# Performance work log

Measured on AMD Instinct MI355X. Metric: run time of the kernel, lower is better.

## Reference

```python
import jax, jax.numpy as jnp
import numpy as np
from jax import lax

VOCAB, HIDDEN, LAYERS = 32000, 1024, 4
DT = 0.1


def setup_inputs() -> dict:
    key = jax.random.key(0)
    ks = jax.random.split(key, 12)
    B, S, H, L, V = 4, 512, HIDDEN, LAYERS, VOCAB
    xav = float(np.sqrt(6.0 / (H + H)))  # xavier_uniform bound for HxH
    # orthogonal-ish fixed W per layer (QR of gaussian)
    g = jax.random.normal(ks[0], (L, H, H), dtype=jnp.float32)
    Ws = jnp.stack([jnp.linalg.qr(g[i])[0] for i in range(L)])
    return {
        "input_ids": jax.random.randint(ks[1], (B, S), 0, V),
        "emb": jax.random.normal(ks[2], (V, H), dtype=jnp.float32) * 0.02,
        "proj_w": jax.random.normal(ks[3], (V, H), dtype=jnp.float32) * 0.02,
        "proj_b": jnp.zeros((V,), dtype=jnp.float32),
        "lambda_param": jnp.float32(0.0),
        "Ws": Ws,
        "Us": jax.random.uniform(ks[4], (L, H, H), jnp.float32, -xav, xav),
        "bs": jnp.zeros((L, H), dtype=jnp.float32),
        "tau_wh": jax.random.uniform(ks[5], (L, H, H), jnp.float32, -xav, xav),
        "tau_wu": jax.random.uniform(ks[6], (L, H, H), jnp.float32, -xav, xav),
        "tau_b": jax.random.uniform(ks[7], (L, H), jnp.float32, -2.0, 2.0),
    }


def reference(input_ids, emb, proj_w, proj_b, lambda_param, Ws, Us, bs, tau_wh, tau_wu, tau_b):
    L = Ws.shape[0]
    B, S = input_ids.shape
    H = emb.shape[1]
    x = emb[input_ids]  # [B, S, H]
    pos_lambda = jax.nn.softplus(lambda_param)

    def step(h, u_t):  # h: [L, B, H], u_t: [B, H]
        layer_in = u_t
        new_h = []
        for i in range(L):
            hp = h[i]
            tau = jax.nn.softplus(hp @ tau_wh[i].T + layer_in @ tau_wu[i].T + tau_b[i]) + 0.01
            tau = lax.stop_gradient(tau)  # torch.no_grad block
            act = jnp.tanh(hp @ Ws[i].T + layer_in @ Us[i].T + bs[i])
            dx = jnp.clip(pos_lambda * (-hp / tau + act), -10.0, 10.0)
            hn = hp + DT * dx
            new_h.append(hn)
            layer_in = hn
        return jnp.stack(new_h), layer_in

    h0 = jnp.zeros((L, B, H), dtype=x.dtype)
    hT, outs = lax.scan(step, h0, jnp.swapaxes(x, 0, 1))  # outs: [S, B, H]
    out_seq = jnp.swapaxes(outs, 0, 1)  # [B, S, H]
    logits = out_seq @ proj_w.T + proj_b  # [B, S, V]
    return logits, hT
```

## Files before the change

kernel.cpp:

```cpp
#include <hip/hip_runtime.h>
#include <hip/hip_bf16.h>

#define NL 4
#define NB 4
#define NS 512
#define NH 1024
#define NV 32000
#define RING 16

typedef unsigned int u32;
typedef unsigned short u16;
typedef __attribute__((ext_vector_type(8))) __bf16 vbf16x8;
typedef __attribute__((ext_vector_type(8))) u16   vu16x8;
typedef __attribute__((ext_vector_type(4))) u32   vu32x4;
typedef __attribute__((ext_vector_type(4))) float vf32x4;

__device__ __forceinline__ u16 f2bf(float f) {
    u32 x = __builtin_bit_cast(u32, f);
    x += 0x7FFFu + ((x >> 16) & 1u);
    return (u16)(x >> 16);
}
__device__ __forceinline__ float softplus_f(float x) {
    return fmaxf(x, 0.0f) + log1pf(expf(-fabsf(x)));
}
__device__ __forceinline__ int aloadi(const int* p) {
    return __hip_atomic_load(p, __ATOMIC_RELAXED, __HIP_MEMORY_SCOPE_AGENT);
}
__device__ __forceinline__ u32 aload32(const u32* p) {
    return __hip_atomic_load(p, __ATOMIC_RELAXED, __HIP_MEMORY_SCOPE_AGENT);
}
__device__ __forceinline__ void astorei(int* p, int v) {
    __hip_atomic_store(p, v, __ATOMIC_RELAXED, __HIP_MEMORY_SCOPE_AGENT);
}
__device__ __forceinline__ void astore32(u32* p, u32 v) {
    __hip_atomic_store(p, v, __ATOMIC_RELAXED, __HIP_MEMORY_SCOPE_AGENT);
}

#define APAD 8
#define ASTR (NH + APAD)

__global__ __launch_bounds__(256, 1) void lnn_recur(
    const int* __restrict__ ids, const float* __restrict__ emb,
    const float* __restrict__ Ws, const float* __restrict__ Us,
    const float* __restrict__ bsv, const float* __restrict__ twh,
    const float* __restrict__ twu, const float* __restrict__ tbv,
    const float* __restrict__ lambda_p,
    int* ack, u32* ring, u16* out16, float* hT_out)
{
    __shared__ __align__(16) u16 act_hp[5][ASTR];
    __shared__ __align__(16) u16 act_in[5][ASTR];
    __shared__ float cross[4][16][4];
    __shared__ float bias_a[16], bias_t[16];

    const int bid   = blockIdx.x;
    const int layer = bid & 3;
    const int slice = bid >> 2;
    const int j0    = slice << 4;
    const int tid   = threadIdx.x;
    const int wave  = tid >> 6;
    const int lane  = tid & 63;

    const float* msel = (wave == 0) ? Ws : (wave == 1) ? Us : (wave == 2) ? twh : twu;
    const float* mat  = msel + (size_t)layer * NH * NH;
    const int jr = j0 + (lane & 15);
    const int kb = (lane >> 4) * 8;
    vbf16x8 wfrag[32];
#pragma unroll
    for (int c = 0; c < 32; ++c) {
        const float* s = mat + (size_t)jr * NH + c * 32 + kb;
        vu16x8 t8;
#pragma unroll
        for (int e = 0; e < 8; ++e) t8[e] = f2bf(s[e]);
        wfrag[c] = __builtin_bit_cast(vbf16x8, t8);
    }

    for (int i = tid; i < ASTR; i += 256) { act_hp[4][i] = 0; act_in[4][i] = 0; }
    if (tid < 16) {
        bias_a[tid] = bsv[layer * NH + j0 + tid];
        bias_t[tid] = tbv[layer * NH + j0 + tid];
    }
    const float lam = softplus_f(lambda_p[0]);
    float hreg = 0.0f;
    const int lm1 = (layer > 0) ? layer - 1 : 0;

    for (int t = 0; t < NS; ++t) {
        {
            const int b = wave;
            const u32* hb_ = ring + (((size_t)(layer * NB + b)) * RING + ((t - 1) & (RING - 1))) * NH + lane;
            const u32* ib_ = ring + (((size_t)(lm1   * NB + b)) * RING + ( t      & (RING - 1))) * NH + lane;
            u32 hv[16], iv[16];
            u32 pendH = (t > 0)     ? 0xFFFFu : 0u;
            u32 pendI = (layer > 0) ? 0xFFFFu : 0u;
            const u32 seqH = (u32)t, seqI = (u32)(t + 1);
            const bool needAck = (wave == 0) && (layer < 3) && (t >= RING);
            const int  ackTgt  = t - RING + 1;
            const int* ackp    = ack + (layer + 1) * 64 + lane;
            bool ackok = !needAck;

            if (t == 0) {
#pragma unroll
                for (int i = 0; i < 16; ++i) hv[i] = 0;
            }
            if (layer == 0) {
                const int v = ids[b * NS + t];
                const float* er = emb + (size_t)v * NH + lane;
#pragma unroll
                for (int i = 0; i < 16; ++i) iv[i] = ((u32)f2bf(er[64 * i])) << 16;
            }
            for (int it = 0; it < (1 << 20); ++it) {
#pragma unroll
                for (int i = 0; i < 16; ++i) if (pendH & (1u << i)) hv[i] = aload32(hb_ + 64 * i);
#pragma unroll
                for (int i = 0; i < 16; ++i) if (pendI & (1u << i)) iv[i] = aload32(ib_ + 64 * i);
#pragma unroll
                for (int i = 0; i < 16; ++i) if ((pendH & (1u << i)) && ((hv[i] & 0xFFFFu) == seqH)) pendH &= ~(1u << i);
#pragma unroll
                for (int i = 0; i < 16; ++i) if ((pendI & (1u << i)) && ((iv[i] & 0xFFFFu) == seqI)) pendI &= ~(1u << i);
                if (needAck && !ackok) ackok = (aloadi(ackp) >= ackTgt);
                const bool done = (pendH == 0u) & (pendI == 0u) & (ackok | !needAck);
                if (__all((int)done)) break;
                __builtin_amdgcn_s_sleep(2);
            }
#pragma unroll
            for (int i = 0; i < 16; ++i) {
                act_hp[b][64 * i + lane] = (u16)(hv[i] >> 16);
                act_in[b][64 * i + lane] = (u16)(iv[i] >> 16);
            }
        }
        __syncthreads();
        if (tid == 0 && layer > 0) astorei(ack + layer * 64 + slice, t + 1);

        {
            const u16 (*asrc)[ASTR] = ((wave & 1) == 0) ? act_hp : act_in;
            int ar = lane & 15; if (ar > 4) ar = 4;
            vf32x4 a0 = {0.f,0.f,0.f,0.f}, a1 = a0, a2 = a0, a3 = a0;
#pragma unroll
            for (int c = 0; c < 32; c += 4) {
                a0 = __builtin_amdgcn_mfma_f32_16x16x32_bf16(*(const vbf16x8*)&asrc[ar][(c+0)*32+kb], wfrag[c+0], a0, 0, 0, 0);
                a1 = __builtin_amdgcn_mfma_f32_16x16x32_bf16(*(const vbf16x8*)&asrc[ar][(c+1)*32+kb], wfrag[c+1], a1, 0, 0, 0);
                a2 = __builtin_amdgcn_mfma_f32_16x16x32_bf16(*(const vbf16x8*)&asrc[ar][(c+2)*32+kb], wfrag[c+2], a2, 0, 0, 0);
                a3 = __builtin_amdgcn_mfma_f32_16x16x32_bf16(*(const vbf16x8*)&asrc[ar][(c+3)*32+kb], wfrag[c+3], a3, 0, 0, 0);
            }
            vf32x4 acc = (a0 + a1) + (a2 + a3);
            if (lane < 16) {
#pragma unroll
                for (int r = 0; r < 4; ++r) cross[wave][lane][r] = acc[r];
            }
        }
        __syncthreads();

        if (wave == 0) {
            const int j = lane & 15, b = lane >> 4;
            const float sa = cross[0][j][b] + cross[1][j][b] + bias_a[j];
            const float st = cross[2][j][b] + cross[3][j][b] + bias_t[j];
            const float tau = softplus_f(st) + 0.01f;
            const float av  = tanhf(sa);
            float dx = lam * (av - hreg / tau);
            dx = fminf(10.0f, fmaxf(-10.0f, dx));
            hreg = fmaf(0.1f, dx, hreg);
            const u16 hb = f2bf(hreg);
            const u32 pk = ((u32)hb << 16) | (u32)(t + 1);
            astore32(ring + (((size_t)(layer * NB + b)) * RING + (t & (RING - 1))) * NH + j0 + j, pk);
            if (layer == 3) out16[((size_t)b * NS + t) * NH + j0 + j] = hb;
            if (t == NS - 1) hT_out[((size_t)layer * NB + b) * NH + j0 + j] = hreg;
        }
    }
}

#define BM 128
#define BN 128
#define BK 32
#define KSTEPS (NH / BK)
#define LSTR (BK + 8)

__global__ __launch_bounds__(256, 1) void proj_gemm(
    const u16* __restrict__ A, const float* __restrict__ Bw,
    const float* __restrict__ bias, float* __restrict__ C)
{
    __shared__ __align__(16) u16 Asm[2][BM][LSTR];
    __shared__ __align__(16) u16 Bsm[2][BN][LSTR];

    const int tid  = threadIdx.x;
    const int wave = tid >> 6, lane = tid & 63;
    const int wr = wave >> 1, wc = wave & 1;

    const int nwg = gridDim.x;
    const int id  = blockIdx.x;
    const int q = nwg >> 3, r = nwg & 7;
    const int x = id & 7, o = id >> 3;
    const int wg = (x < r ? x * (q + 1) : r * (q + 1) + (x - r) * q) + o;
    const int m0 = (wg & 15) * BM;
    const int n0 = (wg >> 4) * BN;

    const int srow  = tid >> 1;
    const int shalf = tid & 1;
    const u16*   agp = A  + (size_t)(m0 + srow) * NH + shalf * 16;
    const float* bgp = Bw + (size_t)(n0 + srow) * NH + shalf * 16;

    vf32x4 zed = {0.f, 0.f, 0.f, 0.f};
    vf32x4 acc[4][4];
#pragma unroll
    for (int m = 0; m < 4; ++m)
#pragma unroll
        for (int n = 0; n < 4; ++n) acc[m][n] = zed;

    vu32x4 areg0, areg1; vf32x4 breg0, breg1, breg2, breg3;
    auto load_tile = [&](int kt) {
        const u16* ap = agp + kt * BK;
        areg0 = *(const vu32x4*)ap;
        areg1 = *(const vu32x4*)(ap + 8);
        const float* bp = bgp + kt * BK;
        breg0 = *(const vf32x4*)bp;       breg1 = *(const vf32x4*)(bp + 4);
        breg2 = *(const vf32x4*)(bp + 8); breg3 = *(const vf32x4*)(bp + 12);
    };
    auto write_tile = [&](int buf) {
        u16* ad = &Asm[buf][srow][shalf * 16];
        *(vu32x4*)ad = areg0; *(vu32x4*)(ad + 8) = areg1;
        float fb[16];
        *(vf32x4*)&fb[0] = breg0; *(vf32x4*)&fb[4]  = breg1;
        *(vf32x4*)&fb[8] = breg2; *(vf32x4*)&fb[12] = breg3;
        vu16x8 v0, v1;
#pragma unroll
        for (int e = 0; e < 8; ++e) { v0[e] = f2bf(fb[e]); v1[e] = f2bf(fb[8 + e]); }
        u16* bd = &Bsm[buf][srow][shalf * 16];
        *(vu16x8*)bd = v0; *(vu16x8*)(bd + 8) = v1;
    };

    load_tile(0); write_tile(0);
    __syncthreads();

    const int fr = lane & 15;
    const int fk = (lane >> 4) * 8;
    for (int kt = 0; kt < KSTEPS; ++kt) {
        const int cur = kt & 1;
        if (kt + 1 < KSTEPS) load_tile(kt + 1);
        vbf16x8 afr[4], bfr[4];
#pragma unroll
        for (int m = 0; m < 4; ++m)
            afr[m] = *(const vbf16x8*)&Asm[cur][wr * 64 + m * 16 + fr][fk];
#pragma unroll
        for (int n = 0; n < 4; ++n)
            bfr[n] = *(const vbf16x8*)&Bsm[cur][wc * 64 + n * 16 + fr][fk];
#pragma unroll
        for (int m = 0; m < 4; ++m)
#pragma unroll
            for (int n = 0; n < 4; ++n)
                acc[m][n] = __builtin_amdgcn_mfma_f32_16x16x32_bf16(afr[m], bfr[n], acc[m][n], 0, 0, 0);
        if (kt + 1 < KSTEPS) write_tile(cur ^ 1);
        __syncthreads();
    }

    const int cc = lane & 15;
    const int cr = (lane >> 4) * 4;
#pragma unroll
    for (int m = 0; m < 4; ++m) {
#pragma unroll
        for (int n = 0; n < 4; ++n) {
            const int gc = n0 + wc * 64 + n * 16 + cc;
            const float bval = bias[gc];
            float* cp = C + (size_t)(m0 + wr * 64 + m * 16 + cr) * NV + gc;
#pragma unroll
            for (int r = 0; r < 4; ++r)
                cp[(size_t)r * NV] = acc[m][n][r] + bval;
        }
    }
}

extern "C" void kernel_launch(void* const* d_in, const int* in_sizes, int n_in,
                              void* d_out, int out_size, void* d_ws, size_t ws_size,
                              hipStream_t stream) {
    const int*   ids = (const int*)  d_in[0];
    const float* emb = (const float*)d_in[1];
    const float* pw  = (const float*)d_in[2];
    const float* pb  = (const float*)d_in[3];
    const float* lam = (const float*)d_in[4];
    const float* Ws  = (const float*)d_in[5];
    const float* Us  = (const float*)d_in[6];
    const float* bsv = (const float*)d_in[7];
    const float* twh = (const float*)d_in[8];
    const float* twu = (const float*)d_in[9];
    const float* tbv = (const float*)d_in[10];

    char* ws = (char*)d_ws;
    u32* ring     = (u32*)ws;
    int* ack      = (int*)(ws + (1 << 20));
    u16* out_bf16 = (u16*)(ws + (1 << 20) + 4096);

    float* logits = (float*)d_out;
    float* hT     = logits + (size_t)NB * NS * NV;

    hipMemsetAsync(ws, 0, (1 << 20) + 4096, stream);
    lnn_recur<<<dim3(256), dim3(256), 0, stream>>>(ids, emb, Ws, Us, bsv, twh, twu, tbv, lam,
                                                   ack, ring, out_bf16, hT);
    proj_gemm<<<dim3((NV / BN) * ((NB * NS) / BM)), dim3(256), 0, stream>>>(out_bf16, pw, pb, logits);
}
```

Measured before the change: 2.809 ms.

## Replace per-element sequence-tagged ring with packed bf16 ring and per-slice flags

```diff
diff --git a/kernel.cpp b/kernel.cpp
--- a/kernel.cpp
+++ b/kernel.cpp
@@ -10,6 +10,7 @@
 
 typedef unsigned int u32;
 typedef unsigned short u16;
+typedef unsigned long long u64;
 typedef __attribute__((ext_vector_type(8))) __bf16 vbf16x8;
 typedef __attribute__((ext_vector_type(8))) u16   vu16x8;
 typedef __attribute__((ext_vector_type(4))) u32   vu32x4;
@@ -26,7 +27,7 @@
 __device__ __forceinline__ int aloadi(const int* p) {
     return __hip_atomic_load(p, __ATOMIC_RELAXED, __HIP_MEMORY_SCOPE_AGENT);
 }
-__device__ __forceinline__ u32 aload32(const u32* p) {
+__device__ __forceinline__ u64 aload64(const u64* p) {
     return __hip_atomic_load(p, __ATOMIC_RELAXED, __HIP_MEMORY_SCOPE_AGENT);
 }
 __device__ __forceinline__ void astorei(int* p, int v) {
@@ -45,7 +46,7 @@
     const float* __restrict__ bsv, const float* __restrict__ twh,
     const float* __restrict__ twu, const float* __restrict__ tbv,
     const float* __restrict__ lambda_p,
-    int* ack, u32* ring, u16* out16, float* hT_out)
+    int* flags, int* ack, u32* ring, u32* out_dw, float* hT_out)
 {
     __shared__ __align__(16) u16 act_hp[5][ASTR];
     __shared__ __align__(16) u16 act_in[5][ASTR];
@@ -84,48 +85,62 @@
     const int lm1 = (layer > 0) ? layer - 1 : 0;
 
     for (int t = 0; t < NS; ++t) {
+        const int b     = wave;
+        const int slotH = (t - 1) & (RING - 1);
+        const int slotI = t & (RING - 1);
+        u64 hq[4], iq[4];
+
+        if (layer == 0) {
+            const int v = ids[b * NS + t];
+            const float* er = emb + (size_t)v * NH;
+#pragma unroll
+            for (int q = 0; q < 4; ++q) {
+                vf32x4 f = *(const vf32x4*)(er + 4 * (lane + 64 * q));
+                u32 lo = (u32)f2bf(f[0]) | ((u32)f2bf(f[1]) << 16);
+                u32 hi = (u32)f2bf(f[2]) | ((u32)f2bf(f[3]) << 16);
+                iq[q] = (u64)lo | ((u64)hi << 32);
+            }
+        }
+
         {
-            const int b = wave;
-            const u32* hb_ = ring + (((size_t)(layer * NB + b)) * RING + ((t - 1) & (RING - 1))) * NH + lane;
-            const u32* ib_ = ring + (((size_t)(lm1   * NB + b)) * RING + ( t      & (RING - 1))) * NH + lane;
-            u32 hv[16], iv[16];
-            u32 pendH = (t > 0)     ? 0xFFFFu : 0u;
-            u32 pendI = (layer > 0) ? 0xFFFFu : 0u;
-            const u32 seqH = (u32)t, seqI = (u32)(t + 1);
-            const bool needAck = (wave == 0) && (layer < 3) && (t >= RING);
+            const bool needH = (t > 0);
+            const bool needI = (layer > 0);
+            const int* fH = flags + ((layer << 4) + slotH) * 64 + lane;
+            const int* fI = flags + ((lm1   << 4) + slotI) * 64 + lane;
+            const bool needAck = (layer < 3) && (t >= RING);
             const int  ackTgt  = t - RING + 1;
             const int* ackp    = ack + (layer + 1) * 64 + lane;
             bool ackok = !needAck;
-
-            if (t == 0) {
-#pragma unroll
-                for (int i = 0; i < 16; ++i) hv[i] = 0;
+            for (int it = 0; it < (1 << 20); ++it) {
+                bool ok = true;
+                if (needH) ok &= (aloadi(fH) >= t);
+                if (needI) ok &= (aloadi(fI) >= t + 1);
+                if (!ackok) ackok = (aloadi(ackp) >= ackTgt);
+                ok &= ackok;
+                if (__all((int)ok)) break;
+                __builtin_amdgcn_s_sleep(1);
             }
-            if (layer == 0) {
-                const int v = ids[b * NS + t];
-                const float* er = emb + (size_t)v * NH + lane;
-#pragma unroll
-                for (int i = 0; i < 16; ++i) iv[i] = ((u32)f2bf(er[64 * i])) << 16;
-            }
-            for (int it = 0; it < (1 << 20); ++it) {
-#pragma unroll
-                for (int i = 0; i < 16; ++i) if (pendH & (1u << i)) hv[i] = aload32(hb_ + 64 * i);
-#pragma unroll
-                for (int i = 0; i < 16; ++i) if (pendI & (1u << i)) iv[i] = aload32(ib_ + 64 * i);
-#pragma unroll
-                for (int i = 0; i < 16; ++i) if ((pendH & (1u << i)) && ((hv[i] & 0xFFFFu) == seqH)) pendH &= ~(1u << i);
-#pragma unroll
-                for (int i = 0; i < 16; ++i) if ((pendI & (1u << i)) && ((iv[i] & 0xFFFFu) == seqI)) pendI &= ~(1u << i);
-                if (needAck && !ackok) ackok = (aloadi(ackp) >= ackTgt);
-                const bool done = (pendH == 0u) & (pendI == 0u) & (ackok | !needAck);
-                if (__all((int)done)) break;
-                __builtin_amdgcn_s_sleep(2);
-            }
-#pragma unroll
-            for (int i = 0; i < 16; ++i) {
-                act_hp[b][64 * i + lane] = (u16)(hv[i] >> 16);
-                act_in[b][64 * i + lane] = (u16)(iv[i] >> 16);
-            }
+        }
+
+        if (layer > 0) {
+            const u64* ir = (const u64*)(ring + (((size_t)(lm1 * NB + b)) * RING + slotI) * 512);
+#pragma unroll
+            for (int q = 0; q < 4; ++q) iq[q] = aload64(ir + lane + 64 * q);
+        }
+        if (t == 0) {
+            hq[0] = hq[1] = hq[2] = hq[3] = 0;
+        } else {
+            const u64* hr = (layer == 3)
+                ? (const u64*)(out_dw + ((size_t)b * NS + (t - 1)) * 512)
+                : (const u64*)(ring + (((size_t)(layer * NB + b)) * RING + slotH) * 512);
+#pragma unroll
+            for (int q = 0; q < 4; ++q) hq[q] = aload64(hr + lane + 64 * q);
+        }
+        {
+            u64* dh = (u64*)&act_hp[b][0];
+            u64* di = (u64*)&act_in[b][0];
+#pragma unroll
+            for (int q = 0; q < 4; ++q) { dh[lane + 64 * q] = hq[q]; di[lane + 64 * q] = iq[q]; }
         }
         __syncthreads();
         if (tid == 0 && layer > 0) astorei(ack + layer * 64 + slice, t + 1);
@@ -150,19 +165,24 @@
         __syncthreads();
 
         if (wave == 0) {
-            const int j = lane & 15, b = lane >> 4;
-            const float sa = cross[0][j][b] + cross[1][j][b] + bias_a[j];
-            const float st = cross[2][j][b] + cross[3][j][b] + bias_t[j];
+            const int j = lane & 15, bb = lane >> 4;
+            const float sa = cross[0][j][bb] + cross[1][j][bb] + bias_a[j];
+            const float st = cross[2][j][bb] + cross[3][j][bb] + bias_t[j];
             const float tau = softplus_f(st) + 0.01f;
             const float av  = tanhf(sa);
             float dx = lam * (av - hreg / tau);
             dx = fminf(10.0f, fmaxf(-10.0f, dx));
             hreg = fmaf(0.1f, dx, hreg);
             const u16 hb = f2bf(hreg);
-            const u32 pk = ((u32)hb << 16) | (u32)(t + 1);
-            astore32(ring + (((size_t)(layer * NB + b)) * RING + (t & (RING - 1))) * NH + j0 + j, pk);
-            if (layer == 3) out16[((size_t)b * NS + t) * NH + j0 + j] = hb;
-            if (t == NS - 1) hT_out[((size_t)layer * NB + b) * NH + j0 + j] = hreg;
+            const u32 up = (u32)__shfl_down((int)hb, 1);
+            const u32 pk = (u32)hb | (up << 16);
+            u32* rowp = (layer == 3)
+                ? out_dw + ((size_t)bb * NS + t) * 512
+                : ring + (((size_t)(layer * NB + bb)) * RING + slotI) * 512;
+            if ((lane & 1) == 0) astore32(rowp + ((j0 + j) >> 1), pk);
+            asm volatile("s_waitcnt vmcnt(0)" ::: "memory");
+            if (lane == 0) astorei(flags + ((layer << 4) + slotI) * 64 + slice, t + 1);
+            if (t == NS - 1) hT_out[((size_t)layer * NB + bb) * NH + j0 + j] = hreg;
         }
     }
 }
@@ -282,15 +302,17 @@
     const float* tbv = (const float*)d_in[10];
 
     char* ws = (char*)d_ws;
-    u32* ring     = (u32*)ws;
-    int* ack      = (int*)(ws + (1 << 20));
-    u16* out_bf16 = (u16*)(ws + (1 << 20) + 4096);
+    int* flags  = (int*)ws;
+    int* ack    = (int*)(ws + 16384);
+    u32* ring   = (u32*)(ws + 20480);
+    u32* out_dw = (u32*)(ws + 20480 + 524288);
 
     float* logits = (float*)d_out;
     float* hT     = logits + (size_t)NB * NS * NV;
 
-    hipMemsetAsync(ws, 0, (1 << 20) + 4096, stream);
+    hipMemsetAsync(ws, 0, 20480, stream);
     lnn_recur<<<dim3(256), dim3(256), 0, stream>>>(ids, emb, Ws, Us, bsv, twh, twu, tbv, lam,
-                                                   ack, ring, out_bf16, hT);
-    proj_gemm<<<dim3((NV / BN) * ((NB * NS) / BM)), dim3(256), 0, stream>>>(out_bf16, pw, pb, logits);
-}
+                                                   flags, ack, ring, out_dw, hT);
+    proj_gemm<<<dim3((NV / BN) * ((NB * NS) / BM)), dim3(256), 0, stream>>>(
+        (const u16*)out_dw, pw, pb, logits);
+}
```

Measured after the change: 3.122 ms. +11.1%, slower.

## Consolidate recurrence into 64 wide blocks of 1024 threads with deeper ring

Applied to the files above, without the earlier changes.

```diff
diff --git a/kernel.cpp b/kernel.cpp
--- a/kernel.cpp
+++ b/kernel.cpp
@@ -6,10 +6,13 @@
 #define NS 512
 #define NH 1024
 #define NV 32000
-#define RING 16
+#define RING 32
+#define SLICES 16
+#define TPB 1024
 
 typedef unsigned int u32;
 typedef unsigned short u16;
+typedef unsigned long long u64;
 typedef __attribute__((ext_vector_type(8))) __bf16 vbf16x8;
 typedef __attribute__((ext_vector_type(8))) u16   vu16x8;
 typedef __attribute__((ext_vector_type(4))) u32   vu32x4;
@@ -39,30 +42,32 @@
 #define APAD 8
 #define ASTR (NH + APAD)
 
-__global__ __launch_bounds__(256, 1) void lnn_recur(
+__global__ __launch_bounds__(TPB, 1) void lnn_recur(
     const int* __restrict__ ids, const float* __restrict__ emb,
     const float* __restrict__ Ws, const float* __restrict__ Us,
     const float* __restrict__ bsv, const float* __restrict__ twh,
     const float* __restrict__ twu, const float* __restrict__ tbv,
     const float* __restrict__ lambda_p,
-    int* ack, u32* ring, u16* out16, float* hT_out)
+    int* ack, u32* ring, u32* out_dw, float* hT_out)
 {
     __shared__ __align__(16) u16 act_hp[5][ASTR];
     __shared__ __align__(16) u16 act_in[5][ASTR];
-    __shared__ float cross[4][16][4];
-    __shared__ float bias_a[16], bias_t[16];
+    __shared__ float cross[4][4][16][4];
+    __shared__ float bias_a[64], bias_t[64];
 
     const int bid   = blockIdx.x;
     const int layer = bid & 3;
     const int slice = bid >> 2;
-    const int j0    = slice << 4;
+    const int j0    = slice << 6;
     const int tid   = threadIdx.x;
     const int wave  = tid >> 6;
     const int lane  = tid & 63;
-
-    const float* msel = (wave == 0) ? Ws : (wave == 1) ? Us : (wave == 2) ? twh : twu;
+    const int m     = wave & 3;
+    const int rg    = wave >> 2;
+
+    const float* msel = (m == 0) ? Ws : (m == 1) ? Us : (m == 2) ? twh : twu;
     const float* mat  = msel + (size_t)layer * NH * NH;
-    const int jr = j0 + (lane & 15);
+    const int jr = j0 + rg * 16 + (lane & 15);
     const int kb = (lane >> 4) * 8;
     vbf16x8 wfrag[32];
 #pragma unroll
@@ -74,8 +79,8 @@
         wfrag[c] = __builtin_bit_cast(vbf16x8, t8);
     }
 
-    for (int i = tid; i < ASTR; i += 256) { act_hp[4][i] = 0; act_in[4][i] = 0; }
-    if (tid < 16) {
+    for (int i = tid; i < ASTR; i += TPB) { act_hp[4][i] = 0; act_in[4][i] = 0; }
+    if (tid < 64) {
         bias_a[tid] = bsv[layer * NH + j0 + tid];
         bias_t[tid] = tbv[layer * NH + j0 + tid];
     }
@@ -83,55 +88,60 @@
     float hreg = 0.0f;
     const int lm1 = (layer > 0) ? layer - 1 : 0;
 
+    const int pb   = tid >> 8;
+    const int pidx = tid & 255;
+
     for (int t = 0; t < NS; ++t) {
+        const int slotH = (t - 1) & (RING - 1);
+        const int slotI = t & (RING - 1);
+        u32 hv[4], iv[4];
+
+        if (layer == 0) {
+            const int v = ids[pb * NS + t];
+            const float* er = emb + (size_t)v * NH + pidx;
+#pragma unroll
+            for (int q = 0; q < 4; ++q) iv[q] = ((u32)f2bf(er[256 * q])) << 16;
+        }
+
         {
-            const int b = wave;
-            const u32* hb_ = ring + (((size_t)(layer * NB + b)) * RING + ((t - 1) & (RING - 1))) * NH + lane;
-            const u32* ib_ = ring + (((size_t)(lm1   * NB + b)) * RING + ( t      & (RING - 1))) * NH + lane;
-            u32 hv[16], iv[16];
-            u32 pendH = (t > 0)     ? 0xFFFFu : 0u;
-            u32 pendI = (layer > 0) ? 0xFFFFu : 0u;
+            const u32* hbase = ring + (((size_t)(layer * NB + pb)) * RING + slotH) * NH + pidx;
+            const u32* ibase = ring + (((size_t)(lm1   * NB + pb)) * RING + slotI) * NH + pidx;
+            u32 pend = (layer > 0) ? 0xFFu : 0x0Fu;
             const u32 seqH = (u32)t, seqI = (u32)(t + 1);
-            const bool needAck = (wave == 0) && (layer < 3) && (t >= RING);
+            const bool needAck = (layer < 3) && (t >= RING) && (lane < SLICES);
             const int  ackTgt  = t - RING + 1;
-            const int* ackp    = ack + (layer + 1) * 64 + lane;
+            const int* ackp    = ack + (layer + 1) * SLICES + (lane & 15);
             bool ackok = !needAck;
-
-            if (t == 0) {
-#pragma unroll
-                for (int i = 0; i < 16; ++i) hv[i] = 0;
-            }
-            if (layer == 0) {
-                const int v = ids[b * NS + t];
-                const float* er = emb + (size_t)v * NH + lane;
-#pragma unroll
-                for (int i = 0; i < 16; ++i) iv[i] = ((u32)f2bf(er[64 * i])) << 16;
-            }
             for (int it = 0; it < (1 << 20); ++it) {
 #pragma unroll
-                for (int i = 0; i < 16; ++i) if (pendH & (1u << i)) hv[i] = aload32(hb_ + 64 * i);
-#pragma unroll
-                for (int i = 0; i < 16; ++i) if (pendI & (1u << i)) iv[i] = aload32(ib_ + 64 * i);
-#pragma unroll
-                for (int i = 0; i < 16; ++i) if ((pendH & (1u << i)) && ((hv[i] & 0xFFFFu) == seqH)) pendH &= ~(1u << i);
-#pragma unroll
-                for (int i = 0; i < 16; ++i) if ((pendI & (1u << i)) && ((iv[i] & 0xFFFFu) == seqI)) pendI &= ~(1u << i);
+                for (int q = 0; q < 4; ++q) if (pend & (1u << q))       hv[q] = aload32(hbase + 256 * q);
+#pragma unroll
+                for (int q = 0; q < 4; ++q) if (pend & (1u << (4 + q))) iv[q] = aload32(ibase + 256 * q);
+#pragma unroll
+                for (int q = 0; q < 4; ++q) if ((pend & (1u << q)) && ((hv[q] & 0xFFFFu) == seqH)) pend &= ~(1u << q);
+#pragma unroll
+                for (int q = 0; q < 4; ++q) if ((pend & (1u << (4 + q))) && ((iv[q] & 0xFFFFu) == seqI)) pend &= ~(1u << (4 + q));
                 if (needAck && !ackok) ackok = (aloadi(ackp) >= ackTgt);
-                const bool done = (pendH == 0u) & (pendI == 0u) & (ackok | !needAck);
+                const bool done = (pend == 0u) & ackok;
                 if (__all((int)done)) break;
-                __builtin_amdgcn_s_sleep(2);
-            }
-#pragma unroll
-            for (int i = 0; i < 16; ++i) {
-                act_hp[b][64 * i + lane] = (u16)(hv[i] >> 16);
-                act_in[b][64 * i + lane] = (u16)(iv[i] >> 16);
+                __builtin_amdgcn_s_sleep(1);
+            }
+        }
+
+        {
+            u16* dh = &act_hp[pb][0];
+            u16* di = &act_in[pb][0];
+#pragma unroll
+            for (int q = 0; q < 4; ++q) {
+                dh[pidx + 256 * q] = (u16)(hv[q] >> 16);
+                di[pidx + 256 * q] = (u16)(iv[q] >> 16);
             }
         }
         __syncthreads();
-        if (tid == 0 && layer > 0) astorei(ack + layer * 64 + slice, t + 1);
+        if (tid == 0 && layer > 0) astorei(ack + layer * SLICES + slice, t + 1);
 
         {
-            const u16 (*asrc)[ASTR] = ((wave & 1) == 0) ? act_hp : act_in;
+            const u16 (*asrc)[ASTR] = ((m & 1) == 0) ? act_hp : act_in;
             int ar = lane & 15; if (ar > 4) ar = 4;
             vf32x4 a0 = {0.f,0.f,0.f,0.f}, a1 = a0, a2 = a0, a3 = a0;
 #pragma unroll
@@ -144,25 +154,30 @@
             vf32x4 acc = (a0 + a1) + (a2 + a3);
             if (lane < 16) {
 #pragma unroll
-                for (int r = 0; r < 4; ++r) cross[wave][lane][r] = acc[r];
+                for (int r = 0; r < 4; ++r) cross[rg][m][lane][r] = acc[r];
             }
         }
         __syncthreads();
 
-        if (wave == 0) {
-            const int j = lane & 15, b = lane >> 4;
-            const float sa = cross[0][j][b] + cross[1][j][b] + bias_a[j];
-            const float st = cross[2][j][b] + cross[3][j][b] + bias_t[j];
+        if (m == 0) {
+            const int j = lane & 15, bb = lane >> 4;
+            const int jg = j0 + rg * 16 + j;
+            const float sa = cross[rg][0][j][bb] + cross[rg][1][j][bb] + bias_a[rg * 16 + j];
+            const float st = cross[rg][2][j][bb] + cross[rg][3][j][bb] + bias_t[rg * 16 + j];
             const float tau = softplus_f(st) + 0.01f;
             const float av  = tanhf(sa);
             float dx = lam * (av - hreg / tau);
             dx = fminf(10.0f, fmaxf(-10.0f, dx));
             hreg = fmaf(0.1f, dx, hreg);
             const u16 hb = f2bf(hreg);
-            const u32 pk = ((u32)hb << 16) | (u32)(t + 1);
-            astore32(ring + (((size_t)(layer * NB + b)) * RING + (t & (RING - 1))) * NH + j0 + j, pk);
-            if (layer == 3) out16[((size_t)b * NS + t) * NH + j0 + j] = hb;
-            if (t == NS - 1) hT_out[((size_t)layer * NB + b) * NH + j0 + j] = hreg;
+            astore32(ring + (((size_t)(layer * NB + bb)) * RING + slotI) * NH + jg,
+                     ((u32)hb << 16) | (u32)(t + 1));
+            if (layer == 3) {
+                const u32 up = (u32)__shfl_down((int)hb, 1);
+                if ((j & 1) == 0)
+                    out_dw[((size_t)bb * NS + t) * 512 + (jg >> 1)] = (u32)hb | (up << 16);
+            }
+            if (t == NS - 1) hT_out[((size_t)layer * NB + bb) * NH + jg] = hreg;
         }
     }
 }
@@ -236,16 +251,16 @@
         if (kt + 1 < KSTEPS) load_tile(kt + 1);
         vbf16x8 afr[4], bfr[4];
 #pragma unroll
-        for (int m = 0; m < 4; ++m)
-            afr[m] = *(const vbf16x8*)&Asm[cur][wr * 64 + m * 16 + fr][fk];
+        for (int mm = 0; mm < 4; ++mm)
+            afr[mm] = *(const vbf16x8*)&Asm[cur][wr * 64 + mm * 16 + fr][fk];
 #pragma unroll
         for (int n = 0; n < 4; ++n)
             bfr[n] = *(const vbf16x8*)&Bsm[cur][wc * 64 + n * 16 + fr][fk];
 #pragma unroll
-        for (int m = 0; m < 4; ++m)
+        for (int mm = 0; mm < 4; ++mm)
 #pragma unroll
             for (int n = 0; n < 4; ++n)
-                acc[m][n] = __builtin_amdgcn_mfma_f32_16x16x32_bf16(afr[m], bfr[n], acc[m][n], 0, 0, 0);
+                acc[mm][n] = __builtin_amdgcn_mfma_f32_16x16x32_bf16(afr[mm], bfr[n], acc[mm][n], 0, 0, 0);
         if (kt + 1 < KSTEPS) write_tile(cur ^ 1);
         __syncthreads();
     }
@@ -253,15 +268,15 @@
     const int cc = lane & 15;
     const int cr = (lane >> 4) * 4;
 #pragma unroll
-    for (int m = 0; m < 4; ++m) {
+    for (int mm = 0; mm < 4; ++mm) {
 #pragma unroll
         for (int n = 0; n < 4; ++n) {
             const int gc = n0 + wc * 64 + n * 16 + cc;
             const float bval = bias[gc];
-            float* cp = C + (size_t)(m0 + wr * 64 + m * 16 + cr) * NV + gc;
+            float* cp = C + (size_t)(m0 + wr * 64 + mm * 16 + cr) * NV + gc;
 #pragma unroll
             for (int r = 0; r < 4; ++r)
-                cp[(size_t)r * NV] = acc[m][n][r] + bval;
+                cp[(size_t)r * NV] = acc[mm][n][r] + bval;
         }
     }
 }
@@ -282,15 +297,16 @@
     const float* tbv = (const float*)d_in[10];
 
     char* ws = (char*)d_ws;
-    u32* ring     = (u32*)ws;
-    int* ack      = (int*)(ws + (1 << 20));
-    u16* out_bf16 = (u16*)(ws + (1 << 20) + 4096);
+    u32* ring   = (u32*)ws;
+    int* ack    = (int*)(ws + (2 << 20));
+    u32* out_dw = (u32*)(ws + (2 << 20) + 4096);
 
     float* logits = (float*)d_out;
     float* hT     = logits + (size_t)NB * NS * NV;
 
-    hipMemsetAsync(ws, 0, (1 << 20) + 4096, stream);
-    lnn_recur<<<dim3(256), dim3(256), 0, stream>>>(ids, emb, Ws, Us, bsv, twh, twu, tbv, lam,
-                                                   ack, ring, out_bf16, hT);
-    proj_gemm<<<dim3((NV / BN) * ((NB * NS) / BM)), dim3(256), 0, stream>>>(out_bf16, pw, pb, logits);
-}
+    hipMemsetAsync(ws, 0, (2 << 20) + 4096, stream);
+    lnn_recur<<<dim3(NL * SLICES), dim3(TPB), 0, stream>>>(ids, emb, Ws, Us, bsv, twh, twu, tbv, lam,
+                                                           ack, ring, out_dw, hT);
+    proj_gemm<<<dim3((NV / BN) * ((NB * NS) / BM)), dim3(256), 0, stream>>>(
+        (const u16*)out_dw, pw, pb, logits);
+}
```

After: 6.087 ms. 2.17x slower.
